# Optimization experiments

Hardware: AMD Instinct MI355X
Metric: run time of the kernel (lower is better)

Reference implementation:

```python
import jax, jax.numpy as jnp
import numpy as np

NEG_SLOPE = 0.01  # torch nn.LeakyReLU default


def setup_inputs() -> dict:
    key = jax.random.key(0)
    ks = jax.random.split(key, 6)
    B, L, C, D = 4, 1024, 128, 64
    return {
        "queries": jax.random.normal(ks[0], (B, L, C), dtype=jnp.float32),
        "keys": jax.random.normal(ks[1], (B, L, C), dtype=jnp.float32),
        "values": jax.random.normal(ks[2], (B, L, C), dtype=jnp.float32),
        "linear_l": jax.random.normal(ks[3], (C, D), dtype=jnp.float32) * 0.05,
        "linear_r": jax.random.normal(ks[4], (C, D), dtype=jnp.float32) * 0.05,
        "a": jax.random.normal(ks[5], (D, 1), dtype=jnp.float32) * 0.05,
    }


def reference(queries, keys, values, linear_l, linear_r, a):
    # keys/values are accepted by the torch forward but unused in its math.
    # g_l, g_r: (B, L, D)
    g_l = jnp.einsum('blc,cd->bld', queries, linear_l)
    g_r = jnp.einsum('blc,cd->bld', queries, linear_r)
    # torch repeat/repeat_interleave + view(b,l,l,-1) yields
    # g_sum[b, x, y] = g_l[b, y] + g_r[b, x]  -> (B, L, L, D)
    g_sum = g_l[:, None, :, :] + g_r[:, :, None, :]
    g_sum = jnp.where(g_sum >= 0, g_sum, NEG_SLOPE * g_sum)  # LeakyReLU
    e = jnp.einsum('bxyd,d->bxy', g_sum, a[:, 0])            # (B, L, L)
    scores = jax.nn.softmax(e, axis=-1)                       # dropout is identity in eval
    y = jnp.einsum('bxy,byd->bxd', scores, g_r)               # (B, L, D)
    return (y, scores)
```

## Files before the change

### kernel.cpp

```cpp
#include <hip/hip_runtime.h>
#include <math.h>

#define LL   1024
#define NROW 4096
#define DD   64
#define CC   128

#define C1H 0.505f
#define C2H 0.495f

typedef short    bf16x8 __attribute__((ext_vector_type(8)));
typedef float    f32x4  __attribute__((ext_vector_type(4)));
typedef _Float16 hf2    __attribute__((ext_vector_type(2)));

#if defined(__has_builtin)
#if __has_builtin(__builtin_amdgcn_fdot2)
#define HAS_FDOT2 1
#endif
#endif

static __device__ __forceinline__ unsigned short bf16rne(float f) {
  unsigned u = __float_as_uint(f);
  u += 0x7fffu + ((u >> 16) & 1u);
  return (unsigned short)(u >> 16);
}

static __device__ __forceinline__ unsigned rflu(unsigned v) {
  return __builtin_amdgcn_readfirstlane(v);
}
static __device__ __forceinline__ float rflf(float v) {
  return __uint_as_float(__builtin_amdgcn_readfirstlane(__float_as_uint(v)));
}

static __device__ __forceinline__ float dot2abs(unsigned glp, unsigned grp,
                                                unsigned ap, float acc) {
  union { unsigned u; hf2 h; } g1, g2, z, av;
  g1.u = glp; g2.u = grp; av.u = ap;
  z.h = g1.h + g2.h;
  z.u &= 0x7fff7fffu;
#ifdef HAS_FDOT2
  return __builtin_amdgcn_fdot2(z.h, av.h, acc, false);
#else
  return fmaf((float)z.h.y, (float)av.h.y,
              fmaf((float)z.h.x, (float)av.h.x, acc));
#endif
}

__global__ __launch_bounds__(256) void k_proj(
    const float* __restrict__ q, const float* __restrict__ Wl,
    const float* __restrict__ Wr, const float* __restrict__ a,
    uint4* __restrict__ glg, _Float16* __restrict__ gr16,
    unsigned short* __restrict__ grTf,
    float* __restrict__ AL, float* __restrict__ AR) {
  const int bl0 = blockIdx.x * 8;
  const int b = bl0 >> 10;
  const int t = threadIdx.x;
  __shared__ __align__(16) float qs[8 * CC];
  __shared__ __align__(16) unsigned short trT[DD][8];
  __shared__ __align__(16) _Float16 trL[8][DD];

  ((float4*)qs)[t] = ((const float4*)(q + (size_t)bl0 * CC))[t];
  __syncthreads();

  const int rr = t >> 6;
  const int d  = t & 63;
  const int r0 = rr * 2, r1 = rr * 2 + 1;
  const float* q0 = qs + r0 * CC;
  const float* q1 = qs + r1 * CC;

  float aL0 = 0, aL1 = 0, aR0 = 0, aR1 = 0;
  float bL0 = 0, bL1 = 0, bR0 = 0, bR1 = 0;
#pragma unroll 8
  for (int c = 0; c < CC; c += 2) {
    float wl0 = Wl[c * DD + d],       wr0 = Wr[c * DD + d];
    float wl1 = Wl[(c + 1) * DD + d], wr1 = Wr[(c + 1) * DD + d];
    aL0 = fmaf(q0[c], wl0, aL0);  bL0 = fmaf(q0[c + 1], wl1, bL0);
    aL1 = fmaf(q1[c], wl0, aL1);  bL1 = fmaf(q1[c + 1], wl1, bL1);
    aR0 = fmaf(q0[c], wr0, aR0);  bR0 = fmaf(q0[c + 1], wr1, bR0);
    aR1 = fmaf(q1[c], wr0, aR1);  bR1 = fmaf(q1[c + 1], wr1, bR1);
  }
  float gL0 = aL0 + bL0, gL1 = aL1 + bL1;
  float gR0 = aR0 + bR0, gR1 = aR1 + bR1;

  trL[r0][d] = (_Float16)gL0;
  trL[r1][d] = (_Float16)gL1;
  gr16[(size_t)(bl0 + r0) * DD + d] = (_Float16)gR0;
  gr16[(size_t)(bl0 + r1) * DD + d] = (_Float16)gR1;
  trT[d][r0] = bf16rne(gR0);
  trT[d][r1] = bf16rne(gR1);

  float av = a[d];
  float vL0 = av * gL0, vL1 = av * gL1, vR0 = av * gR0, vR1 = av * gR1;
#pragma unroll
  for (int off = 1; off < 64; off <<= 1) {
    vL0 += __shfl_xor(vL0, off, 64);
    vL1 += __shfl_xor(vL1, off, 64);
    vR0 += __shfl_xor(vR0, off, 64);
    vR1 += __shfl_xor(vR1, off, 64);
  }
  if (d == 0) {
    AL[bl0 + r0] = vL0; AL[bl0 + r1] = vL1;
    AR[bl0 + r0] = vR0; AR[bl0 + r1] = vR1;
  }
  __syncthreads();
  if (t < 64) {
    const int kc = (bl0 & 1023) >> 5;
    const int hi = ((bl0 & 1023) >> 3) & 3;
    ((uint4*)grTf)[((size_t)((b * 32 + kc) * 4 + (t >> 4)) << 6) +
                   hi * 16 + (t & 15)] = *(const uint4*)&trT[t][0];
  } else if (t < 128) {
    int tt = t - 64;
    int r = tt >> 3, g = tt & 7;
    glg[(((size_t)(b * 8 + g)) << 10) + (bl0 & 1023) + r] =
        *(const uint4*)&trL[r][g * 8];
  }
}

__global__ __launch_bounds__(512, 4) void k_fused(
    const uint4* __restrict__ glg, const _Float16* __restrict__ gr16,
    const unsigned short* __restrict__ grTf,
    const float* __restrict__ AL, const float* __restrict__ AR,
    const float* __restrict__ a,
    float* __restrict__ scores, float* __restrict__ yout) {
  const int bl0 = blockIdx.x * 8;
  const int b = bl0 >> 10;
  const int t = threadIdx.x;
  const int w = t >> 6, l = t & 63;

  __shared__ __align__(16) _Float16 grL[8 * DD];
  __shared__ __align__(16) unsigned short eb[8704];
  __shared__ __align__(16) float sPV[8][4][8][17];
  __shared__ __align__(16) float sSx[8][8];

  uint4 gv[4][2][2];
#pragma unroll
  for (int dblk = 0; dblk < 4; ++dblk)
#pragma unroll
    for (int yc = 0; yc < 2; ++yc)
#pragma unroll
      for (int g2 = 0; g2 < 2; ++g2)
        gv[dblk][yc][g2] =
            glg[(((size_t)(b * 8 + dblk * 2 + g2)) << 10) + yc * 512 + t];

  if (t < 256)
    ((unsigned*)grL)[t] = ((const unsigned*)(gr16 + (size_t)bl0 * DD))[t];

  unsigned sa[32];
#pragma unroll
  for (int k = 0; k < 16; ++k) {
    float4 av = *(const float4*)&a[k * 4];
    union { hf2 h; unsigned u; } u0, u1;
    u0.h.x = (_Float16)av.x; u0.h.y = (_Float16)av.y;
    u1.h.x = (_Float16)av.z; u1.h.y = (_Float16)av.w;
    sa[k * 2]     = rflu(u0.u);
    sa[k * 2 + 1] = rflu(u1.u);
  }

  float pr[8];
#pragma unroll
  for (int x = 0; x < 8; ++x) pr[x] = C1H * rflf(AR[bl0 + x]);

  float alv[2];
  alv[0] = AL[b * LL + t];
  alv[1] = AL[b * LL + 512 + t];

  float pacc[8][2];
#pragma unroll
  for (int x = 0; x < 8; ++x) { pacc[x][0] = 0.f; pacc[x][1] = 0.f; }

  __syncthreads();

#pragma unroll
  for (int dblk = 0; dblk < 4; ++dblk) {
#pragma unroll
    for (int x = 0; x < 8; ++x) {
      uint4 gra = *(const uint4*)&grL[x * DD + dblk * 16];
      uint4 grb = *(const uint4*)&grL[x * DD + dblk * 16 + 8];
#pragma unroll
      for (int yc = 0; yc < 2; ++yc) {
        float s = pacc[x][yc];
        s = dot2abs(gv[dblk][yc][0].x, gra.x, sa[dblk * 8 + 0], s);
        s = dot2abs(gv[dblk][yc][0].y, gra.y, sa[dblk * 8 + 1], s);
        s = dot2abs(gv[dblk][yc][0].z, gra.z, sa[dblk * 8 + 2], s);
        s = dot2abs(gv[dblk][yc][0].w, gra.w, sa[dblk * 8 + 3], s);
        s = dot2abs(gv[dblk][yc][1].x, grb.x, sa[dblk * 8 + 4], s);
        s = dot2abs(gv[dblk][yc][1].y, grb.y, sa[dblk * 8 + 5], s);
        s = dot2abs(gv[dblk][yc][1].z, grb.z, sa[dblk * 8 + 6], s);
        s = dot2abs(gv[dblk][yc][1].w, grb.w, sa[dblk * 8 + 7], s);
        pacc[x][yc] = s;
      }
    }
  }

  float ev[8][2], lsum[8];
#pragma unroll
  for (int x = 0; x < 8; ++x) {
    ev[x][0] = __expf(fmaf(C2H, pacc[x][0], pr[x] + C1H * alv[0]));
    ev[x][1] = __expf(fmaf(C2H, pacc[x][1], pr[x] + C1H * alv[1]));
    lsum[x] = ev[x][0] + ev[x][1];
  }
#pragma unroll
  for (int off = 1; off < 64; off <<= 1) {
#pragma unroll
    for (int x = 0; x < 8; ++x) lsum[x] += __shfl_xor(lsum[x], off, 64);
  }
  if (l == 0) {
#pragma unroll
    for (int x = 0; x < 8; ++x) sSx[x][w] = lsum[x];
  }
  __syncthreads();

  float isv[8];
#pragma unroll
  for (int x = 0; x < 8; ++x) {
    float4 s0 = *(const float4*)&sSx[x][0];
    float4 s1 = *(const float4*)&sSx[x][4];
    isv[x] = 1.0f / (((s0.x + s0.y) + (s0.z + s0.w)) +
                     ((s1.x + s1.y) + (s1.z + s1.w)));
  }

#pragma unroll
  for (int yc = 0; yc < 2; ++yc) {
    int y = yc * 512 + t;
    int kc = y >> 5, k32 = t & 31;
#pragma unroll
    for (int x = 0; x < 8; ++x) {
      float p = ev[x][yc] * isv[x];
      __builtin_nontemporal_store(p, &scores[((size_t)(bl0 + x) << 10) + y]);
      eb[kc * 256 + x * 32 + k32] = bf16rne(p);
    }
  }
  __syncthreads();

  f32x4 acc[4] = {{0.f, 0.f, 0.f, 0.f}, {0.f, 0.f, 0.f, 0.f},
                  {0.f, 0.f, 0.f, 0.f}, {0.f, 0.f, 0.f, 0.f}};
  const int row16 = l & 15, hh = l >> 4;
#pragma unroll
  for (int kk = 0; kk < 4; ++kk) {
    int kc = w * 4 + kk;
    bf16x8 af = *(const bf16x8*)&eb[kc * 256 + row16 * 32 + hh * 8];
#pragma unroll
    for (int nt = 0; nt < 4; ++nt) {
      bf16x8 bfv = *(const bf16x8*)(grTf +
          ((((size_t)((b * 32 + kc) * 4 + nt)) << 6) + l) * 8);
      acc[nt] = __builtin_amdgcn_mfma_f32_16x16x32_bf16(af, bfv, acc[nt], 0, 0, 0);
    }
  }
  if (l < 32) {
#pragma unroll
    for (int nt = 0; nt < 4; ++nt)
#pragma unroll
      for (int i = 0; i < 4; ++i)
        sPV[w][nt][hh * 4 + i][row16] = acc[nt][i];
  }
  __syncthreads();
  {
    int x = t >> 6, dcol = t & 63, nt = dcol >> 4, col = dcol & 15;
    float r = 0.f;
#pragma unroll
    for (int ww = 0; ww < 8; ++ww) r += sPV[ww][nt][x][col];
    yout[(size_t)(bl0 + x) * DD + dcol] = r;
  }
}

extern "C" void kernel_launch(void* const* d_in, const int* in_sizes, int n_in,
                              void* d_out, int out_size, void* d_ws, size_t ws_size,
                              hipStream_t stream) {
  const float* q  = (const float*)d_in[0];
  const float* Wl = (const float*)d_in[3];
  const float* Wr = (const float*)d_in[4];
  const float* a  = (const float*)d_in[5];

  float* yout = (float*)d_out;
  float* esc  = yout + NROW * DD;

  float* ws = (float*)d_ws;
  float* AL = ws;
  float* AR = AL + NROW;
  uint4* glg = (uint4*)(AR + NROW);
  _Float16* gr16 = (_Float16*)(glg + (size_t)NROW * 8);
  unsigned short* grTf = (unsigned short*)(gr16 + (size_t)NROW * DD);

  k_proj <<<NROW / 8, 256, 0, stream>>>(q, Wl, Wr, a, glg, gr16, grTf, AL, AR);
  k_fused<<<NROW / 8, 512, 0, stream>>>(glg, gr16, grTf, AL, AR, a, esc, yout);
}
```

Baseline: 34.23 us.

## Use 1024 threads per block so each thread handles one key column

The fused attention kernel now launches 1024 threads per block instead of 512. Each thread processes a single key position rather than two, which halves the per-thread register arrays for gathered g_l values, partial scores and exponentials. The PV MFMA work is split over 16 waves instead of 8, and the cross-wave reduction buffers and row-sum combine are widened to match. The goal is more latency hiding and lower register pressure, at the cost of more syncthreads overhead and a larger final reduction across waves.

Result: slower. 35.15 us (+2.7%).

```diff
diff --git a/kernel.cpp b/kernel.cpp
--- a/kernel.cpp
+++ b/kernel.cpp
@@ -116,7 +116,7 @@
   }
 }
 
-__global__ __launch_bounds__(512, 4) void k_fused(
+__global__ __launch_bounds__(1024, 8) void k_fused(
     const uint4* __restrict__ glg, const _Float16* __restrict__ gr16,
     const unsigned short* __restrict__ grTf,
     const float* __restrict__ AL, const float* __restrict__ AR,
@@ -129,18 +129,8 @@
 
   __shared__ __align__(16) _Float16 grL[8 * DD];
   __shared__ __align__(16) unsigned short eb[8704];
-  __shared__ __align__(16) float sPV[8][4][8][17];
-  __shared__ __align__(16) float sSx[8][8];
-
-  uint4 gv[4][2][2];
-#pragma unroll
-  for (int dblk = 0; dblk < 4; ++dblk)
-#pragma unroll
-    for (int yc = 0; yc < 2; ++yc)
-#pragma unroll
-      for (int g2 = 0; g2 < 2; ++g2)
-        gv[dblk][yc][g2] =
-            glg[(((size_t)(b * 8 + dblk * 2 + g2)) << 10) + yc * 512 + t];
+  __shared__ __align__(16) float sPV[16][4][8][17];
+  __shared__ __align__(16) float sSx[8][16];
 
   if (t < 256)
     ((unsigned*)grL)[t] = ((const unsigned*)(gr16 + (size_t)bl0 * DD))[t];
@@ -160,44 +150,40 @@
 #pragma unroll
   for (int x = 0; x < 8; ++x) pr[x] = C1H * rflf(AR[bl0 + x]);
 
-  float alv[2];
-  alv[0] = AL[b * LL + t];
-  alv[1] = AL[b * LL + 512 + t];
-
-  float pacc[8][2];
-#pragma unroll
-  for (int x = 0; x < 8; ++x) { pacc[x][0] = 0.f; pacc[x][1] = 0.f; }
+  const float alv = AL[b * LL + t];
+
+  float pacc[8];
+#pragma unroll
+  for (int x = 0; x < 8; ++x) pacc[x] = 0.f;
 
   __syncthreads();
 
 #pragma unroll
   for (int dblk = 0; dblk < 4; ++dblk) {
+    uint4 gv0 = glg[(((size_t)(b * 8 + dblk * 2 + 0)) << 10) + t];
+    uint4 gv1 = glg[(((size_t)(b * 8 + dblk * 2 + 1)) << 10) + t];
 #pragma unroll
     for (int x = 0; x < 8; ++x) {
       uint4 gra = *(const uint4*)&grL[x * DD + dblk * 16];
       uint4 grb = *(const uint4*)&grL[x * DD + dblk * 16 + 8];
-#pragma unroll
-      for (int yc = 0; yc < 2; ++yc) {
-        float s = pacc[x][yc];
-        s = dot2abs(gv[dblk][yc][0].x, gra.x, sa[dblk * 8 + 0], s);
-        s = dot2abs(gv[dblk][yc][0].y, gra.y, sa[dblk * 8 + 1], s);
-        s = dot2abs(gv[dblk][yc][0].z, gra.z, sa[dblk * 8 + 2], s);
-        s = dot2abs(gv[dblk][yc][0].w, gra.w, sa[dblk * 8 + 3], s);
-        s = dot2abs(gv[dblk][yc][1].x, grb.x, sa[dblk * 8 + 4], s);
-        s = dot2abs(gv[dblk][yc][1].y, grb.y, sa[dblk * 8 + 5], s);
-        s = dot2abs(gv[dblk][yc][1].z, grb.z, sa[dblk * 8 + 6], s);
-        s = dot2abs(gv[dblk][yc][1].w, grb.w, sa[dblk * 8 + 7], s);
-        pacc[x][yc] = s;
-      }
+      float s = pacc[x];
+      s = dot2abs(gv0.x, gra.x, sa[dblk * 8 + 0], s);
+      s = dot2abs(gv0.y, gra.y, sa[dblk * 8 + 1], s);
+      s = dot2abs(gv0.z, gra.z, sa[dblk * 8 + 2], s);
+      s = dot2abs(gv0.w, gra.w, sa[dblk * 8 + 3], s);
+      s = dot2abs(gv1.x, grb.x, sa[dblk * 8 + 4], s);
+      s = dot2abs(gv1.y, grb.y, sa[dblk * 8 + 5], s);
+      s = dot2abs(gv1.z, grb.z, sa[dblk * 8 + 6], s);
+      s = dot2abs(gv1.w, grb.w, sa[dblk * 8 + 7], s);
+      pacc[x] = s;
     }
   }
 
-  float ev[8][2], lsum[8];
+  float ev[8], lsum[8];
 #pragma unroll
   for (int x = 0; x < 8; ++x) {
-    ev[x][0] = __expf(fmaf(C2H, pacc[x][0], pr[x] + C1H * alv[0]));
-    ev[x][1] = __expf(fmaf(C2H, pacc[x][1], pr[x] + C1H * alv[1]));
-    lsum[x] = ev[x][0] + ev[x][1];
+    ev[x] = __expf(fmaf(C2H, pacc[x], pr[x] + C1H * alv));
+    lsum[x] = ev[x];
   }
 #pragma unroll
   for (int off = 1; off < 64; off <<= 1) {
@@ -215,18 +201,20 @@
   for (int x = 0; x < 8; ++x) {
     float4 s0 = *(const float4*)&sSx[x][0];
     float4 s1 = *(const float4*)&sSx[x][4];
-    isv[x] = 1.0f / (((s0.x + s0.y) + (s0.z + s0.w)) +
-                     ((s1.x + s1.y) + (s1.z + s1.w)));
-  }
-
-#pragma unroll
-  for (int yc = 0; yc < 2; ++yc) {
-    int y = yc * 512 + t;
-    int kc = y >> 5, k32 = t & 31;
+    float4 s2 = *(const float4*)&sSx[x][8];
+    float4 s3 = *(const float4*)&sSx[x][12];
+    isv[x] = 1.0f / ((((s0.x + s0.y) + (s0.z + s0.w)) +
+                      ((s1.x + s1.y) + (s1.z + s1.w))) +
+                     (((s2.x + s2.y) + (s2.z + s2.w)) +
+                      ((s3.x + s3.y) + (s3.z + s3.w))));
+  }
+
+  {
+    const int kc = t >> 5, k32 = t & 31;
 #pragma unroll
     for (int x = 0; x < 8; ++x) {
-      float p = ev[x][yc] * isv[x];
-      __builtin_nontemporal_store(p, &scores[((size_t)(bl0 + x) << 10) + y]);
+      float p = ev[x] * isv[x];
+      __builtin_nontemporal_store(p, &scores[((size_t)(bl0 + x) << 10) + t]);
       eb[kc * 256 + x * 32 + k32] = bf16rne(p);
     }
   }
@@ -236,8 +224,8 @@
                   {0.f, 0.f, 0.f, 0.f}, {0.f, 0.f, 0.f, 0.f}};
   const int row16 = l & 15, hh = l >> 4;
 #pragma unroll
-  for (int kk = 0; kk < 4; ++kk) {
-    int kc = w * 4 + kk;
+  for (int kk = 0; kk < 2; ++kk) {
+    int kc = w * 2 + kk;
     bf16x8 af = *(const bf16x8*)&eb[kc * 256 + row16 * 32 + hh * 8];
 #pragma unroll
     for (int nt = 0; nt < 4; ++nt) {
@@ -254,11 +242,11 @@
         sPV[w][nt][hh * 4 + i][row16] = acc[nt][i];
   }
   __syncthreads();
-  {
+  if (t < 512) {
     int x = t >> 6, dcol = t & 63, nt = dcol >> 4, col = dcol & 15;
     float r = 0.f;
 #pragma unroll
-    for (int ww = 0; ww < 8; ++ww) r += sPV[ww][nt][x][col];
+    for (int ww = 0; ww < 16; ++ww) r += sPV[ww][nt][x][col];
     yout[(size_t)(bl0 + x) * DD + dcol] = r;
   }
 }
@@ -282,5 +270,5 @@
   unsigned short* grTf = (unsigned short*)(gr16 + (size_t)NROW * DD);
 
   k_proj <<<NROW / 8, 256, 0, stream>>>(q, Wl, Wr, a, glg, gr16, grTf, AL, AR);
-  k_fused<<<NROW / 8, 512, 0, stream>>>(glg, gr16, grTf, AL, AR, a, esc, yout);
-}
+  k_fused<<<NROW / 8, 1024, 0, stream>>>(glg, gr16, grTf, AL, AR, a, esc, yout);
+}
```
